# Optimization experiments

Hardware: AMD Instinct MI355X
Metric: run time of the kernel (lower is better)

Reference implementation:

```python
import jax, jax.numpy as jnp
import numpy as np

H = 1024
T = 4096


def _lstm_layer(x, w_ih, w_hh, b_ih, b_hh):
    """Single unidirectional LSTM layer, batch=1. x: [T, in]. Returns [T, H].
    PyTorch gate order: i, f, g, o."""
    # Precompute input contributions for all timesteps in one GEMM: [T, 4H]
    gx_all = x @ w_ih.T + (b_ih + b_hh)
    w_hh_t = w_hh.T  # [H, 4H]

    def step(carry, gx):
        h, c = carry                      # each [H]
        g = gx + h @ w_hh_t               # [4H]
        i, f, gg, o = jnp.split(g, 4)
        i = jax.nn.sigmoid(i)
        f = jax.nn.sigmoid(f)
        o = jax.nn.sigmoid(o)
        c = f * c + i * jnp.tanh(gg)
        h = o * jnp.tanh(c)
        return (h, c), h

    h0 = jnp.zeros((w_hh.shape[1],), dtype=x.dtype)
    c0 = jnp.zeros_like(h0)
    _, hs = jax.lax.scan(step, (h0, c0), gx_all)
    return hs  # [T, H]


def setup_inputs() -> dict:
    key = jax.random.key(0)
    ks = jax.random.split(key, 9)
    s = 1.0 / np.sqrt(H)  # PyTorch LSTM init scale
    return {
        "x": jax.random.normal(ks[0], (T, H), dtype=jnp.float32),
        "w_ih0": jax.random.normal(ks[1], (4 * H, H), dtype=jnp.float32) * s,
        "w_hh0": jax.random.normal(ks[2], (4 * H, H), dtype=jnp.float32) * s,
        "b_ih0": jax.random.normal(ks[3], (4 * H,), dtype=jnp.float32) * s,
        "b_hh0": jax.random.normal(ks[4], (4 * H,), dtype=jnp.float32) * s,
        "w_ih1": jax.random.normal(ks[5], (4 * H, H), dtype=jnp.float32) * s,
        "w_hh1": jax.random.normal(ks[6], (4 * H, H), dtype=jnp.float32) * s,
        "b_ih1": jax.random.normal(ks[7], (4 * H,), dtype=jnp.float32) * s,
        "b_hh1": jax.random.normal(ks[8], (4 * H,), dtype=jnp.float32) * s,
    }


def reference(x, w_ih0, w_hh0, b_ih0, b_hh0, w_ih1, w_hh1, b_ih1, b_hh1):
    # 2-layer LSTM with zero initial (h, c); output is top layer's hidden
    # sequence, matching output.squeeze(1) in the torch module.
    h1 = _lstm_layer(x, w_ih0, w_hh0, b_ih0, b_hh0)
    h2 = _lstm_layer(h1, w_ih1, w_hh1, b_ih1, b_hh1)
    return h2  # [T, H]
```

## Files before the change

### kernel.cpp

```cpp
#include <hip/hip_runtime.h>

#define HH 1024
#define TT 4096
#define NWG 256
#define NWG_PER_LAYER 128
#define JS_PER_WG 8
#define JS_PER_WAVE 2
#define LDS_BYTES 131072

__device__ __forceinline__ float fsigmoid(float x) {
    return 1.0f / (1.0f + __expf(-x));
}
__device__ __forceinline__ float ftanh(float x) {
    float ax = fabsf(x);
    float e = __expf(-2.0f * ax);
    float t = (1.0f - e) / (1.0f + e);
    return copysignf(t, x);
}
__device__ __forceinline__ void fma4(float& a, const float4 w, const float4 v) {
    a = fmaf(w.x, v.x, a);
    a = fmaf(w.y, v.y, a);
    a = fmaf(w.z, v.z, a);
    a = fmaf(w.w, v.w, a);
}

__device__ __forceinline__ void load64B_llc(float4 v[4], const float* p) {
    asm volatile(
        "global_load_dwordx4 %0, %4, off sc0 sc1\n\t"
        "global_load_dwordx4 %1, %4, off offset:16 sc0 sc1\n\t"
        "global_load_dwordx4 %2, %4, off offset:32 sc0 sc1\n\t"
        "global_load_dwordx4 %3, %4, off offset:48 sc0 sc1\n\t"
        "s_waitcnt vmcnt(0)"
        : "=&v"(v[0]), "=&v"(v[1]), "=&v"(v[2]), "=&v"(v[3])
        : "v"(p)
        : "memory");
}

__device__ __forceinline__ void slot_barrier_wait(const unsigned* slots, unsigned tgt) {
    const unsigned* p = slots + 4 * (threadIdx.x & 63);
    for (;;) {
        uint4 v;
        asm volatile(
            "global_load_dwordx4 %0, %1, off sc0 sc1\n\t"
            "s_waitcnt vmcnt(0)"
            : "=&v"(v) : "v"(p) : "memory");
        const unsigned m = min(min(v.x, v.y), min(v.z, v.w));
        if (__all(m >= tgt)) break;
        __builtin_amdgcn_s_sleep(1);
    }
}

#define FOR_R(F) F(0) F(1) F(2) F(3) F(4) F(5) F(6) F(7)

__global__ __launch_bounds__(256, 1) void lstm2_persistent(
    const float* __restrict__ x,
    const float* __restrict__ wih0, const float* __restrict__ whh0,
    const float* __restrict__ bih0, const float* __restrict__ bhh0,
    const float* __restrict__ wih1, const float* __restrict__ whh1,
    const float* __restrict__ bih1, const float* __restrict__ bhh1,
    float* __restrict__ out,
    float* __restrict__ ring,
    const float* __restrict__ zbuf,
    unsigned* __restrict__ slots)
{
    extern __shared__ float ldsw[];

    const int wg   = blockIdx.x;
    const int tid  = threadIdx.x;
    const int wave = tid >> 6;
    const int lane = tid & 63;
    const bool isL1 = (wg >= NWG_PER_LAYER);
    const int wgl   = isL1 ? (wg - NWG_PER_LAYER) : wg;
    const int jbase = wgl * JS_PER_WG + wave * JS_PER_WAVE;
    const int col   = lane * 16;

    const float* wih = isL1 ? wih1 : wih0;
    const float* whh = isL1 ? whh1 : whh0;
    const float* bih = isL1 ? bih1 : bih0;
    const float* bhh = isL1 ? bhh1 : bhh0;

    #pragma unroll
    for (int r = 0; r < 8; ++r) {
        const int row = (r & 3) * HH + (jbase + (r >> 2));
        const float4* p  = (const float4*)(whh + (size_t)row * HH + col);
        float*       wb = ldsw + wave * 8192 + r * 1024 + lane * 4;
        #pragma unroll
        for (int q = 0; q < 4; ++q)
            *(float4*)(wb + q * 256) = p[q];
    }

    #define DECLA(r) float AI##r##_0, AI##r##_1, AI##r##_2,  AI##r##_3, \
                           AI##r##_4, AI##r##_5, AI##r##_6,  AI##r##_7, \
                           AI##r##_8, AI##r##_9, AI##r##_10, AI##r##_11, \
                           AI##r##_12, AI##r##_13, AI##r##_14, AI##r##_15;
    FOR_R(DECLA)

    #define AW(dst, s) asm volatile("v_accvgpr_write_b32 %0, %1" : "=a"(dst) : "v"(s));
    #define AWI(r) { \
        const int row = ((r) & 3) * HH + (jbase + ((r) >> 2)); \
        const float4* pw = (const float4*)(wih + (size_t)row * HH + col); \
        float4 w0 = pw[0], w1 = pw[1], w2 = pw[2], w3 = pw[3]; \
        AW(AI##r##_0,  w0.x) AW(AI##r##_1,  w0.y) AW(AI##r##_2,  w0.z) AW(AI##r##_3,  w0.w) \
        AW(AI##r##_4,  w1.x) AW(AI##r##_5,  w1.y) AW(AI##r##_6,  w1.z) AW(AI##r##_7,  w1.w) \
        AW(AI##r##_8,  w2.x) AW(AI##r##_9,  w2.y) AW(AI##r##_10, w2.z) AW(AI##r##_11, w2.w) \
        AW(AI##r##_12, w3.x) AW(AI##r##_13, w3.y) AW(AI##r##_14, w3.z) AW(AI##r##_15, w3.w) }
    FOR_R(AWI)

    #define DECLB(r) float B##r; { const int row = ((r)&3)*HH + (jbase + ((r)>>2)); \
                                   B##r = bih[row] + bhh[row]; }
    FOR_R(DECLB)

    #define DECLG(r) float gxp##r = 0.0f;
    FOR_R(DECLG)

    float c0v = 0.0f, c1v = 0.0f;
    int loff = wave * 8192 + lane * 4;

    #define ARD(src) { asm("v_accvgpr_read_b32 %0, %1" \
                           : "=v"(tt) : "a"(src), "v"(kd)); }
    #define GXA(r) { float a = 0.0f; float tt; \
        ARD(AI##r##_0)  a = fmaf(tt, iv4[0].x, a); \
        ARD(AI##r##_1)  a = fmaf(tt, iv4[0].y, a); \
        ARD(AI##r##_2)  a = fmaf(tt, iv4[0].z, a); \
        ARD(AI##r##_3)  a = fmaf(tt, iv4[0].w, a); \
        ARD(AI##r##_4)  a = fmaf(tt, iv4[1].x, a); \
        ARD(AI##r##_5)  a = fmaf(tt, iv4[1].y, a); \
        ARD(AI##r##_6)  a = fmaf(tt, iv4[1].z, a); \
        ARD(AI##r##_7)  a = fmaf(tt, iv4[1].w, a); \
        ARD(AI##r##_8)  a = fmaf(tt, iv4[2].x, a); \
        ARD(AI##r##_9)  a = fmaf(tt, iv4[2].y, a); \
        ARD(AI##r##_10) a = fmaf(tt, iv4[2].z, a); \
        ARD(AI##r##_11) a = fmaf(tt, iv4[2].w, a); \
        ARD(AI##r##_12) a = fmaf(tt, iv4[3].x, a); \
        ARD(AI##r##_13) a = fmaf(tt, iv4[3].y, a); \
        ARD(AI##r##_14) a = fmaf(tt, iv4[3].z, a); \
        ARD(AI##r##_15) a = fmaf(tt, iv4[3].w, a); \
        gxp##r = a; }

    if (!isL1) {
        float4 iv4[4];
        const float4* p = (const float4*)(x + col);
        iv4[0] = p[0]; iv4[1] = p[1]; iv4[2] = p[2]; iv4[3] = p[3];
        int kd = 0;
        FOR_R(GXA)
    }

    __syncthreads();

    for (int k = 0; k <= TT + 1; ++k) {
        asm volatile("" : "+v"(loff));

        const int t = isL1 ? (k - 2) : k;

        if (t >= 0 && t < TT) {
            float4 hp4[4];
            const float* hpv = (t > 0)
                ? (isL1 ? out + (size_t)(t - 1) * HH : ring + (size_t)((t - 1) & 3) * HH)
                : zbuf;
            load64B_llc(hp4, hpv + col);

            float acc0, acc1, acc2, acc3, acc4, acc5, acc6, acc7;
            #define DOTW(r) { float a = gxp##r; \
                const float4* wp = (const float4*)(ldsw + loff + (r) * 1024); \
                fma4(a, wp[0],   hp4[0]); fma4(a, wp[64],  hp4[1]); \
                fma4(a, wp[128], hp4[2]); fma4(a, wp[192], hp4[3]); \
                acc##r = a; }
            FOR_R(DOTW)

            #define REDW(m) \
                acc0 += __shfl_xor(acc0, m, 64); acc1 += __shfl_xor(acc1, m, 64); \
                acc2 += __shfl_xor(acc2, m, 64); acc3 += __shfl_xor(acc3, m, 64); \
                acc4 += __shfl_xor(acc4, m, 64); acc5 += __shfl_xor(acc5, m, 64); \
                acc6 += __shfl_xor(acc6, m, 64); acc7 += __shfl_xor(acc7, m, 64);
            REDW(1) REDW(2) REDW(4) REDW(8) REDW(16) REDW(32)

            const float gi0 = fsigmoid(acc0 + B0), gf0 = fsigmoid(acc1 + B1);
            const float gg0 = ftanh(acc2 + B2),    go0 = fsigmoid(acc3 + B3);
            c0v = gf0 * c0v + gi0 * gg0;
            const float h0 = go0 * ftanh(c0v);
            const float gi1 = fsigmoid(acc4 + B4), gf1 = fsigmoid(acc5 + B5);
            const float gg1 = ftanh(acc6 + B6),    go1 = fsigmoid(acc7 + B7);
            c1v = gf1 * c1v + gi1 * gg1;
            const float h1v = go1 * ftanh(c1v);

            if (lane == 0) {
                float2 hv = make_float2(h0, h1v);
                unsigned long long bits;
                __builtin_memcpy(&bits, &hv, 8);
                float* dstf = isL1 ? (out  + (size_t)t * HH + jbase)
                                   : (ring + (size_t)(t & 3) * HH + jbase);
                __hip_atomic_store((unsigned long long*)dstf, bits,
                                   __ATOMIC_RELAXED, __HIP_MEMORY_SCOPE_AGENT);
            }
        }

        __syncthreads();

        if (k <= TT) {
            if (tid == 0) {
                asm volatile("s_waitcnt vmcnt(0)" ::: "memory");
                __hip_atomic_store(&slots[wg], (unsigned)(k + 1),
                                   __ATOMIC_RELAXED, __HIP_MEMORY_SCOPE_AGENT);
            }

            {
                const int tn = t + 1;
                if (tn >= 0 && tn < TT) {
                    float4 iv4[4];
                    if (!isL1) {
                        const float4* p = (const float4*)(x + (size_t)tn * HH + col);
                        iv4[0] = p[0]; iv4[1] = p[1]; iv4[2] = p[2]; iv4[3] = p[3];
                    } else {
                        load64B_llc(iv4, ring + (size_t)(tn & 3) * HH + col);
                    }
                    int kd = k;
                    FOR_R(GXA)
                }
            }
            asm volatile("" : "+v"(gxp0), "+v"(gxp1), "+v"(gxp2), "+v"(gxp3),
                             "+v"(gxp4), "+v"(gxp5), "+v"(gxp6), "+v"(gxp7));

            slot_barrier_wait(slots, (unsigned)(k + 1));
        }
    }
}

extern "C" void kernel_launch(void* const* d_in, const int* in_sizes, int n_in,
                              void* d_out, int out_size, void* d_ws, size_t ws_size,
                              hipStream_t stream) {
    (void)in_sizes; (void)n_in; (void)out_size; (void)ws_size;
    const float* x    = (const float*)d_in[0];
    const float* wih0 = (const float*)d_in[1];
    const float* whh0 = (const float*)d_in[2];
    const float* bih0 = (const float*)d_in[3];
    const float* bhh0 = (const float*)d_in[4];
    const float* wih1 = (const float*)d_in[5];
    const float* whh1 = (const float*)d_in[6];
    const float* bih1 = (const float*)d_in[7];
    const float* bhh1 = (const float*)d_in[8];
    float* out = (float*)d_out;

    unsigned* slots = (unsigned*)d_ws;
    float*    zbuf  = (float*)((char*)d_ws + 4096);
    float*    ring  = (float*)((char*)d_ws + 8192);

    (void)hipFuncSetAttribute((const void*)lstm2_persistent,
                              hipFuncAttributeMaxDynamicSharedMemorySize, LDS_BYTES);

    (void)hipMemsetAsync(d_ws, 0, 24576, stream);

    hipLaunchKernelGGL(lstm2_persistent, dim3(NWG), dim3(256), LDS_BYTES, stream,
                       x, wih0, whh0, bih0, bhh0,
                       wih1, whh1, bih1, bhh1, out, ring, zbuf, slots);
}
```

Measured before the change: 15.48 ms.

## Use eight waves per workgroup with one hidden unit per wave

Doubles the workgroup to 512 threads so each wave owns a single hidden unit (four gate rows) instead of two. Per-wave work on the serial critical path is halved: half the LDS dot products, shuffle reductions and activations per step. The cost is more waves contending for the same CU, more per-block __syncthreads overhead, and AGPR/VGPR pressure under the 512-thread launch bound.

```diff
diff --git a/kernel.cpp b/kernel.cpp
--- a/kernel.cpp
+++ b/kernel.cpp
@@ -5,7 +5,7 @@
 #define NWG 256
 #define NWG_PER_LAYER 128
 #define JS_PER_WG 8
-#define JS_PER_WAVE 2
+#define NTHREADS 512
 #define LDS_BYTES 131072
 
 __device__ __forceinline__ float fsigmoid(float x) {
@@ -50,9 +50,9 @@
     }
 }
 
-#define FOR_R(F) F(0) F(1) F(2) F(3) F(4) F(5) F(6) F(7)
-
-__global__ __launch_bounds__(256, 1) void lstm2_persistent(
+#define FOR_R(F) F(0) F(1) F(2) F(3)
+
+__global__ __launch_bounds__(NTHREADS, 1) void lstm2_persistent(
     const float* __restrict__ x,
     const float* __restrict__ wih0, const float* __restrict__ whh0,
     const float* __restrict__ bih0, const float* __restrict__ bhh0,
@@ -71,7 +71,7 @@
     const int lane = tid & 63;
     const bool isL1 = (wg >= NWG_PER_LAYER);
     const int wgl   = isL1 ? (wg - NWG_PER_LAYER) : wg;
-    const int jbase = wgl * JS_PER_WG + wave * JS_PER_WAVE;
+    const int jb    = wgl * JS_PER_WG + wave;
     const int col   = lane * 16;
 
     const float* wih = isL1 ? wih1 : wih0;
@@ -80,10 +80,10 @@
     const float* bhh = isL1 ? bhh1 : bhh0;
 
     #pragma unroll
-    for (int r = 0; r < 8; ++r) {
-        const int row = (r & 3) * HH + (jbase + (r >> 2));
+    for (int r = 0; r < 4; ++r) {
+        const int row = r * HH + jb;
         const float4* p  = (const float4*)(whh + (size_t)row * HH + col);
-        float*       wb = ldsw + wave * 8192 + r * 1024 + lane * 4;
+        float*       wb = ldsw + wave * 4096 + r * 1024 + lane * 4;
         #pragma unroll
         for (int q = 0; q < 4; ++q)
             *(float4*)(wb + q * 256) = p[q];
@@ -97,7 +97,7 @@
 
     #define AW(dst, s) asm volatile("v_accvgpr_write_b32 %0, %1" : "=a"(dst) : "v"(s));
     #define AWI(r) { \
-        const int row = ((r) & 3) * HH + (jbase + ((r) >> 2)); \
+        const int row = (r) * HH + jb; \
         const float4* pw = (const float4*)(wih + (size_t)row * HH + col); \
         float4 w0 = pw[0], w1 = pw[1], w2 = pw[2], w3 = pw[3]; \
         AW(AI##r##_0,  w0.x) AW(AI##r##_1,  w0.y) AW(AI##r##_2,  w0.z) AW(AI##r##_3,  w0.w) \
@@ -106,15 +106,15 @@
         AW(AI##r##_12, w3.x) AW(AI##r##_13, w3.y) AW(AI##r##_14, w3.z) AW(AI##r##_15, w3.w) }
     FOR_R(AWI)
 
-    #define DECLB(r) float B##r; { const int row = ((r)&3)*HH + (jbase + ((r)>>2)); \
+    #define DECLB(r) float B##r; { const int row = (r) * HH + jb; \
                                    B##r = bih[row] + bhh[row]; }
     FOR_R(DECLB)
 
     #define DECLG(r) float gxp##r = 0.0f;
     FOR_R(DECLG)
 
-    float c0v = 0.0f, c1v = 0.0f;
-    int loff = wave * 8192 + lane * 4;
+    float cv = 0.0f;
+    int loff = wave * 4096 + lane * 4;
 
     #define ARD(src) { asm("v_accvgpr_read_b32 %0, %1" \
                            : "=v"(tt) : "a"(src), "v"(kd)); }
@@ -159,7 +159,7 @@
                 : zbuf;
             load64B_llc(hp4, hpv + col);
 
-            float acc0, acc1, acc2, acc3, acc4, acc5, acc6, acc7;
+            float acc0, acc1, acc2, acc3;
             #define DOTW(r) { float a = gxp##r; \
                 const float4* wp = (const float4*)(ldsw + loff + (r) * 1024); \
                 fma4(a, wp[0],   hp4[0]); fma4(a, wp[64],  hp4[1]); \
@@ -169,27 +169,18 @@
 
             #define REDW(m) \
                 acc0 += __shfl_xor(acc0, m, 64); acc1 += __shfl_xor(acc1, m, 64); \
-                acc2 += __shfl_xor(acc2, m, 64); acc3 += __shfl_xor(acc3, m, 64); \
-                acc4 += __shfl_xor(acc4, m, 64); acc5 += __shfl_xor(acc5, m, 64); \
-                acc6 += __shfl_xor(acc6, m, 64); acc7 += __shfl_xor(acc7, m, 64);
+                acc2 += __shfl_xor(acc2, m, 64); acc3 += __shfl_xor(acc3, m, 64);
             REDW(1) REDW(2) REDW(4) REDW(8) REDW(16) REDW(32)
 
-            const float gi0 = fsigmoid(acc0 + B0), gf0 = fsigmoid(acc1 + B1);
-            const float gg0 = ftanh(acc2 + B2),    go0 = fsigmoid(acc3 + B3);
-            c0v = gf0 * c0v + gi0 * gg0;
-            const float h0 = go0 * ftanh(c0v);
-            const float gi1 = fsigmoid(acc4 + B4), gf1 = fsigmoid(acc5 + B5);
-            const float gg1 = ftanh(acc6 + B6),    go1 = fsigmoid(acc7 + B7);
-            c1v = gf1 * c1v + gi1 * gg1;
-            const float h1v = go1 * ftanh(c1v);
+            const float gi = fsigmoid(acc0 + B0), gf = fsigmoid(acc1 + B1);
+            const float gg = ftanh(acc2 + B2),    go = fsigmoid(acc3 + B3);
+            cv = gf * cv + gi * gg;
+            const float h = go * ftanh(cv);
 
             if (lane == 0) {
-                float2 hv = make_float2(h0, h1v);
-                unsigned long long bits;
-                __builtin_memcpy(&bits, &hv, 8);
-                float* dstf = isL1 ? (out  + (size_t)t * HH + jbase)
-                                   : (ring + (size_t)(t & 3) * HH + jbase);
-                __hip_atomic_store((unsigned long long*)dstf, bits,
+                float* dstf = isL1 ? (out  + (size_t)t * HH + jb)
+                                   : (ring + (size_t)(t & 3) * HH + jb);
+                __hip_atomic_store((unsigned*)dstf, __float_as_uint(h),
                                    __ATOMIC_RELAXED, __HIP_MEMORY_SCOPE_AGENT);
             }
         }
@@ -217,8 +208,7 @@
                     FOR_R(GXA)
                 }
             }
-            asm volatile("" : "+v"(gxp0), "+v"(gxp1), "+v"(gxp2), "+v"(gxp3),
-                             "+v"(gxp4), "+v"(gxp5), "+v"(gxp6), "+v"(gxp7));
+            asm volatile("" : "+v"(gxp0), "+v"(gxp1), "+v"(gxp2), "+v"(gxp3));
 
             slot_barrier_wait(slots, (unsigned)(k + 1));
         }
@@ -249,7 +239,7 @@
 
     (void)hipMemsetAsync(d_ws, 0, 24576, stream);
 
-    hipLaunchKernelGGL(lstm2_persistent, dim3(NWG), dim3(256), LDS_BYTES, stream,
+    hipLaunchKernelGGL(lstm2_persistent, dim3(NWG), dim3(NTHREADS), LDS_BYTES, stream,
                        x, wih0, whh0, bih0, bhh0,
                        wih1, whh1, bih1, bhh1, out, ring, zbuf, slots);
 }
```

Measured after the change: 16.02 ms. 3.5% more time.
